# Performance work log

Hardware: AMD Instinct MI355X
Metric: run time of the kernel (lower is better)

## Reference

```python
import jax, jax.numpy as jnp
import numpy as np

HEADS = 16
ROT_DIM = 32  # RotaryEmbedding(dim=32), interleaved (GPT-J style) as in rotary_embedding_torch
THETA = 10000.0


def _rope(x):
    # x: (B, H, S, hd); rotate first ROT_DIM dims, pass through the rest
    S = x.shape[-2]
    inv_freq = 1.0 / (THETA ** (jnp.arange(0, ROT_DIM, 2, dtype=jnp.float32) / ROT_DIM))  # (ROT_DIM/2,)
    ang = jnp.arange(S, dtype=jnp.float32)[:, None] * inv_freq[None, :]                   # (S, ROT_DIM/2)
    ang = jnp.repeat(ang, 2, axis=-1)                                                     # (S, ROT_DIM) interleaved
    cos, sin = jnp.cos(ang), jnp.sin(ang)
    xr, xp = x[..., :ROT_DIM], x[..., ROT_DIM:]
    # rotate_half, interleaved pairs: (x1, x2) -> (-x2, x1)
    x2 = xr.reshape(*xr.shape[:-1], ROT_DIM // 2, 2)
    xr_half = jnp.stack([-x2[..., 1], x2[..., 0]], axis=-1).reshape(xr.shape)
    xr = xr * cos + xr_half * sin
    return jnp.concatenate([xr, xp], axis=-1)


def _split_heads(x, H):
    # (S, B, D) -> (B, H, S, hd)
    S, B, D = x.shape
    return x.transpose(1, 0, 2).reshape(B, S, H, D // H).transpose(0, 2, 1, 3)


def setup_inputs() -> dict:
    key = jax.random.key(0)
    ks = jax.random.split(key, 11)
    S, B, D = 2048, 2, 1024
    f = lambda k, shp, s=1.0: jax.random.normal(k, shp, dtype=jnp.float32) * s
    return {
        "Q": f(ks[0], (S, B, D)),
        "K": f(ks[1], (S, B, D)),
        "V": f(ks[2], (S, B, D)),
        "Wq": f(ks[3], (D, D), 0.02), "bq": f(ks[4], (D,), 0.02),
        "Wk": f(ks[5], (D, D), 0.02), "bk": f(ks[6], (D,), 0.02),
        "Wv": f(ks[7], (D, D), 0.02), "bv": f(ks[8], (D,), 0.02),
        "Wo": f(ks[9], (D, D), 0.02), "bo": f(ks[10], (D,), 0.02),
    }


def reference(Q, K, V, Wq, bq, Wk, bk, Wv, bv, Wo, bo):
    S, B, D = Q.shape
    H = HEADS
    hd = D // H
    q = _rope(_split_heads(Q @ Wq.T + bq, H))   # (B, H, S, hd)
    k = _rope(_split_heads(K @ Wk.T + bk, H))
    v = _split_heads(V @ Wv.T + bv, H)
    scores = jnp.einsum("bhqd,bhkd->bhqk", q, k) / jnp.sqrt(jnp.float32(hd))
    probs = jax.nn.softmax(scores, axis=-1)
    out = jnp.einsum("bhqk,bhkd->bhqd", probs, v)  # (B, H, S, hd)
    out = out.transpose(0, 2, 1, 3).reshape(B, S, D).transpose(1, 0, 2)  # (S, B, D)
    return out @ Wo.T + bo
```

## Files before the change

kernel.cpp:

```cpp
#include <hip/hip_runtime.h>
#include <hip/hip_bf16.h>
#include <hip/hip_fp16.h>

#define S_LEN  2048
#define BATCH  2
#define DMODEL 1024
#define NHEADS 16
#define HD     64
#define MROWS  4096
#define LD     72

using f16 = _Float16;
typedef __attribute__((ext_vector_type(8))) _Float16 f16x8;
typedef __attribute__((ext_vector_type(4))) _Float16 f16x4;
typedef __attribute__((ext_vector_type(4))) float    f32x4;

__device__ __forceinline__ void gload16(const void* g, void* l)
{
    __builtin_amdgcn_global_load_lds((const __attribute__((address_space(1))) void*)g,
                                     (__attribute__((address_space(3))) void*)l, 16, 0, 0);
}

__global__ __launch_bounds__(256) void rope_table(float* __restrict__ rc, float* __restrict__ rs)
{
    int idx = blockIdx.x * 256 + threadIdx.x;
    int s = idx >> 4, i = idx & 15;
    float inv = powf(10000.0f, -(float)(2 * i) / 32.0f);
    float ang = (float)s * inv;
    rc[idx] = cosf(ang);
    rs[idx] = sinf(ang);
}

__global__ __launch_bounds__(256) void cvt_all(
    const float* __restrict__ Q, const float* __restrict__ K, const float* __restrict__ V,
    const float* __restrict__ Wq, const float* __restrict__ Wk, const float* __restrict__ Wv,
    const float* __restrict__ Wo, f16* __restrict__ dst)
{
    const int z = blockIdx.y;
    const float* src; size_t off; int n8;
    switch (z) {
        case 0:  src = Q;  off = 0;        n8 = 524288; break;
        case 1:  src = K;  off = 4194304;  n8 = 524288; break;
        case 2:  src = V;  off = 8388608;  n8 = 524288; break;
        case 3:  src = Wq; off = 12582912; n8 = 131072; break;
        case 4:  src = Wk; off = 13631488; n8 = 131072; break;
        case 5:  src = Wv; off = 14680064; n8 = 131072; break;
        default: src = Wo; off = 15728640; n8 = 131072; break;
    }
    int i = blockIdx.x * 256 + threadIdx.x;
    if (i >= n8) return;
    const float4* s = reinterpret_cast<const float4*>(src) + (size_t)i * 2;
    float4 v0 = s[0], v1 = s[1];
    f16x8 h = { (f16)v0.x, (f16)v0.y, (f16)v0.z, (f16)v0.w,
                (f16)v1.x, (f16)v1.y, (f16)v1.z, (f16)v1.w };
    reinterpret_cast<f16x8*>(dst + off)[i] = h;
}

__global__ __launch_bounds__(256) void proj_gemm_h(
    const f16* __restrict__ Xq, const f16* __restrict__ Xk, const f16* __restrict__ Xv,
    const f16* __restrict__ Wq, const f16* __restrict__ Wk, const f16* __restrict__ Wv,
    const float* __restrict__ bq, const float* __restrict__ bk, const float* __restrict__ bv,
    f16* __restrict__ qo, f16* __restrict__ ko, f16* __restrict__ vo,
    const float* __restrict__ rc, const float* __restrict__ rs)
{
    const int mode = blockIdx.z;
    const f16* X     = (mode == 0) ? Xq : (mode == 1) ? Xk : Xv;
    const f16* W     = (mode == 0) ? Wq : (mode == 1) ? Wk : Wv;
    const float* bias = (mode == 0) ? bq : (mode == 1) ? bk : bv;

    __shared__ f16 Al[128 * 32];
    __shared__ f16 Bl[128 * 32];

    const int t = threadIdx.x, lane = t & 63, wid = t >> 6;
    const int q15 = lane & 15, g = lane >> 4;
    const int wr = wid >> 1, wc = wid & 1;
    const int m0 = blockIdx.x * 128, n0 = blockIdx.y * 128;

    const int srow = wid * 16 + (lane >> 2);
    const int scol = (lane & 3) * 8;
    const f16* Xg = X + (size_t)(m0 + srow) * DMODEL + scol;
    const f16* Wg = W + (size_t)(n0 + srow) * DMODEL + scol;
    f16* al0 = &Al[(wid * 16) * 32];
    f16* al1 = &Al[(wid * 16 + 64) * 32];
    f16* bl0 = &Bl[(wid * 16) * 32];
    f16* bl1 = &Bl[(wid * 16 + 64) * 32];

    f32x4 acc[4][4];
    #pragma unroll
    for (int m = 0; m < 4; m++)
        #pragma unroll
        for (int n = 0; n < 4; n++)
            acc[m][n] = f32x4{0.f, 0.f, 0.f, 0.f};

    for (int k0 = 0; k0 < DMODEL; k0 += 32) {
        __syncthreads();
        gload16(Xg + k0, al0);
        gload16(Xg + (size_t)64 * DMODEL + k0, al1);
        gload16(Wg + k0, bl0);
        gload16(Wg + (size_t)64 * DMODEL + k0, bl1);
        __syncthreads();

        f16x8 a[4], b[4];
        #pragma unroll
        for (int m = 0; m < 4; m++)
            a[m] = *reinterpret_cast<const f16x8*>(&Al[(wr * 64 + m * 16 + q15) * 32 + g * 8]);
        #pragma unroll
        for (int n = 0; n < 4; n++)
            b[n] = *reinterpret_cast<const f16x8*>(&Bl[(wc * 64 + n * 16 + q15) * 32 + g * 8]);
        #pragma unroll
        for (int m = 0; m < 4; m++)
            #pragma unroll
            for (int n = 0; n < 4; n++)
                acc[m][n] = __builtin_amdgcn_mfma_f32_16x16x32_f16(a[m], b[n], acc[m][n], 0, 0, 0);
    }

    const int rowb = m0 + wr * 64, colb = n0 + wc * 64;
    #pragma unroll
    for (int n = 0; n < 4; n++) {
        int cN = colb + n * 16 + q15;
        float bvv = bias[cN];
        int h = cN >> 6, d = cN & 63;
        #pragma unroll
        for (int m = 0; m < 4; m++) {
            #pragma unroll
            for (int rg = 0; rg < 4; rg++) {
                int r = rowb + m * 16 + g * 4 + rg;
                int s = r >> 1, bi = r & 1;
                float val = acc[m][n][rg] + bvv;
                if (mode < 2) {
                    float pv = __shfl_xor(val, 1);
                    if (d < 32) {
                        int fi = d >> 1;
                        float cc = rc[s * 16 + fi], ss = rs[s * 16 + fi];
                        val = ((d & 1) == 0) ? val * cc - pv * ss : val * cc + pv * ss;
                    }
                    if (mode == 0) val *= 0.18033688f;
                    ((mode == 0) ? qo : ko)[(((size_t)bi * NHEADS + h) * S_LEN + s) * HD + d] = (f16)val;
                } else {
                    vo[(((size_t)bi * NHEADS + h) * HD + d) * S_LEN + s] = (f16)val;
                }
            }
        }
    }
}

__global__ __launch_bounds__(256) void out_gemm_h(
    const f16* __restrict__ X, const f16* __restrict__ W,
    const float* __restrict__ bias, float* __restrict__ out)
{
    __shared__ f16 Al[128 * 32];
    __shared__ f16 Bl[128 * 32];

    const int t = threadIdx.x, lane = t & 63, wid = t >> 6;
    const int q15 = lane & 15, g = lane >> 4;
    const int wr = wid >> 1, wc = wid & 1;
    const int m0 = blockIdx.x * 128, n0 = blockIdx.y * 128;

    const int srow = wid * 16 + (lane >> 2);
    const int scol = (lane & 3) * 8;
    const f16* Xg = X + (size_t)(m0 + srow) * DMODEL + scol;
    const f16* Wg = W + (size_t)(n0 + srow) * DMODEL + scol;
    f16* al0 = &Al[(wid * 16) * 32];
    f16* al1 = &Al[(wid * 16 + 64) * 32];
    f16* bl0 = &Bl[(wid * 16) * 32];
    f16* bl1 = &Bl[(wid * 16 + 64) * 32];

    f32x4 acc[4][4];
    #pragma unroll
    for (int m = 0; m < 4; m++)
        #pragma unroll
        for (int n = 0; n < 4; n++)
            acc[m][n] = f32x4{0.f, 0.f, 0.f, 0.f};

    for (int k0 = 0; k0 < DMODEL; k0 += 32) {
        __syncthreads();
        gload16(Xg + k0, al0);
        gload16(Xg + (size_t)64 * DMODEL + k0, al1);
        gload16(Wg + k0, bl0);
        gload16(Wg + (size_t)64 * DMODEL + k0, bl1);
        __syncthreads();

        f16x8 a[4], b[4];
        #pragma unroll
        for (int m = 0; m < 4; m++)
            a[m] = *reinterpret_cast<const f16x8*>(&Al[(wr * 64 + m * 16 + q15) * 32 + g * 8]);
        #pragma unroll
        for (int n = 0; n < 4; n++)
            b[n] = *reinterpret_cast<const f16x8*>(&Bl[(wc * 64 + n * 16 + q15) * 32 + g * 8]);
        #pragma unroll
        for (int m = 0; m < 4; m++)
            #pragma unroll
            for (int n = 0; n < 4; n++)
                acc[m][n] = __builtin_amdgcn_mfma_f32_16x16x32_f16(a[m], b[n], acc[m][n], 0, 0, 0);
    }

    const int rowb = m0 + wr * 64, colb = n0 + wc * 64;
    #pragma unroll
    for (int n = 0; n < 4; n++) {
        int cN = colb + n * 16 + q15;
        float bvv = bias[cN];
        #pragma unroll
        for (int m = 0; m < 4; m++) {
            #pragma unroll
            for (int rg = 0; rg < 4; rg++) {
                int r = rowb + m * 16 + g * 4 + rg;
                out[(size_t)r * DMODEL + cN] = acc[m][n][rg] + bvv;
            }
        }
    }
}

__global__ __launch_bounds__(256) void proj_gemm(
    const float* __restrict__ Xq, const float* __restrict__ Xk, const float* __restrict__ Xv,
    const float* __restrict__ Wq, const float* __restrict__ Wk, const float* __restrict__ Wv,
    const float* __restrict__ bq, const float* __restrict__ bk, const float* __restrict__ bv,
    f16* __restrict__ qo, f16* __restrict__ ko, f16* __restrict__ vo,
    const float* __restrict__ rc, const float* __restrict__ rs)
{
    const int mode = blockIdx.z;
    const float* X    = (mode == 0) ? Xq : (mode == 1) ? Xk : Xv;
    const float* W    = (mode == 0) ? Wq : (mode == 1) ? Wk : Wv;
    const float* bias = (mode == 0) ? bq : (mode == 1) ? bk : bv;

    __shared__ f16 Al[128 * 40];
    __shared__ f16 Bl[128 * 40];

    const int t = threadIdx.x;
    const int lane = t & 63, wid = t >> 6;
    const int wr = wid >> 1, wc = wid & 1;
    const int m0 = blockIdx.x * 128, n0 = blockIdx.y * 128;

    f32x4 acc[4][4];
    #pragma unroll
    for (int m = 0; m < 4; m++)
        #pragma unroll
        for (int n = 0; n < 4; n++)
            acc[m][n] = f32x4{0.f, 0.f, 0.f, 0.f};

    for (int k0 = 0; k0 < DMODEL; k0 += 32) {
        __syncthreads();
        #pragma unroll
        for (int i = 0; i < 2; i++) {
            int e = (i * 256 + t) * 8;
            int r = e >> 5, c = e & 31;
            {
                const float* src = &X[(size_t)(m0 + r) * DMODEL + k0 + c];
                float4 v0 = *reinterpret_cast<const float4*>(src);
                float4 v1 = *reinterpret_cast<const float4*>(src + 4);
                f16x8 h = { (f16)v0.x, (f16)v0.y, (f16)v0.z, (f16)v0.w,
                            (f16)v1.x, (f16)v1.y, (f16)v1.z, (f16)v1.w };
                *reinterpret_cast<f16x8*>(&Al[r * 40 + c]) = h;
            }
            {
                const float* src = &W[(size_t)(n0 + r) * DMODEL + k0 + c];
                float4 v0 = *reinterpret_cast<const float4*>(src);
                float4 v1 = *reinterpret_cast<const float4*>(src + 4);
                f16x8 h = { (f16)v0.x, (f16)v0.y, (f16)v0.z, (f16)v0.w,
                            (f16)v1.x, (f16)v1.y, (f16)v1.z, (f16)v1.w };
                *reinterpret_cast<f16x8*>(&Bl[r * 40 + c]) = h;
            }
        }
        __syncthreads();
        f16x8 a[4], b[4];
        #pragma unroll
        for (int m = 0; m < 4; m++)
            a[m] = *reinterpret_cast<const f16x8*>(&Al[(wr * 64 + m * 16 + (lane & 15)) * 40 + (lane >> 4) * 8]);
        #pragma unroll
        for (int n = 0; n < 4; n++)
            b[n] = *reinterpret_cast<const f16x8*>(&Bl[(wc * 64 + n * 16 + (lane & 15)) * 40 + (lane >> 4) * 8]);
        #pragma unroll
        for (int m = 0; m < 4; m++)
            #pragma unroll
            for (int n = 0; n < 4; n++)
                acc[m][n] = __builtin_amdgcn_mfma_f32_16x16x32_f16(a[m], b[n], acc[m][n], 0, 0, 0);
    }

    const int rowb = m0 + wr * 64, colb = n0 + wc * 64;
    #pragma unroll
    for (int n = 0; n < 4; n++) {
        int cN = colb + n * 16 + (lane & 15);
        float bvv = bias[cN];
        int h = cN >> 6, d = cN & 63;
        #pragma unroll
        for (int m = 0; m < 4; m++) {
            #pragma unroll
            for (int rg = 0; rg < 4; rg++) {
                int r = rowb + m * 16 + (lane >> 4) * 4 + rg;
                int s = r >> 1, bi = r & 1;
                float val = acc[m][n][rg] + bvv;
                if (mode < 2) {
                    float pv = __shfl_xor(val, 1);
                    if (d < 32) {
                        int fi = d >> 1;
                        float cc = rc[s * 16 + fi], ss = rs[s * 16 + fi];
                        val = ((d & 1) == 0) ? val * cc - pv * ss : val * cc + pv * ss;
                    }
                    if (mode == 0) val *= 0.18033688f;
                    ((mode == 0) ? qo : ko)[(((size_t)bi * NHEADS + h) * S_LEN + s) * HD + d] = (f16)val;
                } else {
                    vo[(((size_t)bi * NHEADS + h) * HD + d) * S_LEN + s] = (f16)val;
                }
            }
        }
    }
}

__global__ __launch_bounds__(256) void out_gemm(
    const f16* __restrict__ X, const float* __restrict__ W,
    const float* __restrict__ bias, float* __restrict__ out)
{
    __shared__ f16 Al[128 * 40];
    __shared__ f16 Bl[128 * 40];

    const int t = threadIdx.x;
    const int lane = t & 63, wid = t >> 6;
    const int wr = wid >> 1, wc = wid & 1;
    const int m0 = blockIdx.x * 128, n0 = blockIdx.y * 128;

    f32x4 acc[4][4];
    #pragma unroll
    for (int m = 0; m < 4; m++)
        #pragma unroll
        for (int n = 0; n < 4; n++)
            acc[m][n] = f32x4{0.f, 0.f, 0.f, 0.f};

    for (int k0 = 0; k0 < DMODEL; k0 += 32) {
        __syncthreads();
        #pragma unroll
        for (int i = 0; i < 2; i++) {
            int e = (i * 256 + t) * 8;
            int r = e >> 5, c = e & 31;
            *reinterpret_cast<uint4*>(&Al[r * 40 + c]) =
                *reinterpret_cast<const uint4*>(&X[(size_t)(m0 + r) * DMODEL + k0 + c]);
            {
                const float* src = &W[(size_t)(n0 + r) * DMODEL + k0 + c];
                float4 v0 = *reinterpret_cast<const float4*>(src);
                float4 v1 = *reinterpret_cast<const float4*>(src + 4);
                f16x8 h = { (f16)v0.x, (f16)v0.y, (f16)v0.z, (f16)v0.w,
                            (f16)v1.x, (f16)v1.y, (f16)v1.z, (f16)v1.w };
                *reinterpret_cast<f16x8*>(&Bl[r * 40 + c]) = h;
            }
        }
        __syncthreads();
        f16x8 a[4], b[4];
        #pragma unroll
        for (int m = 0; m < 4; m++)
            a[m] = *reinterpret_cast<const f16x8*>(&Al[(wr * 64 + m * 16 + (lane & 15)) * 40 + (lane >> 4) * 8]);
        #pragma unroll
        for (int n = 0; n < 4; n++)
            b[n] = *reinterpret_cast<const f16x8*>(&Bl[(wc * 64 + n * 16 + (lane & 15)) * 40 + (lane >> 4) * 8]);
        #pragma unroll
        for (int m = 0; m < 4; m++)
            #pragma unroll
            for (int n = 0; n < 4; n++)
                acc[m][n] = __builtin_amdgcn_mfma_f32_16x16x32_f16(a[m], b[n], acc[m][n], 0, 0, 0);
    }

    const int rowb = m0 + wr * 64, colb = n0 + wc * 64;
    #pragma unroll
    for (int n = 0; n < 4; n++) {
        int cN = colb + n * 16 + (lane & 15);
        float bvv = bias[cN];
        #pragma unroll
        for (int m = 0; m < 4; m++) {
            #pragma unroll
            for (int rg = 0; rg < 4; rg++) {
                int r = rowb + m * 16 + (lane >> 4) * 4 + rg;
                out[(size_t)r * DMODEL + cN] = acc[m][n][rg] + bvv;
            }
        }
    }
}

__global__ __launch_bounds__(512) void attn_fwd(
    const f16* __restrict__ qb, const f16* __restrict__ kb,
    const f16* __restrict__ vt, f16* __restrict__ ctx)
{
    __shared__ f16 Kl[2][64 * 64];
    __shared__ f16 Vl[2][64 * 64];
    __shared__ f16 Pl[8 * 16 * LD];

    const int t = threadIdx.x, lane = t & 63, wid = t >> 6;
    const int q15 = lane & 15, g = lane >> 4;
    const int sw = q15 & 7;
    const int bh = blockIdx.y;
    const int q0 = blockIdx.x * 128 + wid * 16;

    const f16* qptr = qb + ((size_t)bh * S_LEN + q0) * HD;
    f16x8 qf0 = *reinterpret_cast<const f16x8*>(&qptr[q15 * HD + g * 8]);
    f16x8 qf1 = *reinterpret_cast<const f16x8*>(&qptr[q15 * HD + g * 8 + 32]);

    f32x4 ctxa[4];
    #pragma unroll
    for (int i = 0; i < 4; i++) ctxa[i] = f32x4{0.f, 0.f, 0.f, 0.f};
    float mrun = -3.0e38f, lrun = 0.f;

    const int srow = t >> 3;
    const int sslot = (t & 7) ^ (srow & 7);
    const f16* kg = kb + (size_t)bh * S_LEN * HD + (size_t)srow * HD + sslot * 8;
    const f16* vg = vt + (size_t)bh * HD * S_LEN + (size_t)srow * S_LEN + sslot * 8;
    const int lds_wbase = wid * 512;
    f16* pbase = &Pl[wid * (16 * LD)];

    gload16(kg, &Kl[0][lds_wbase]);
    gload16(vg, &Vl[0][lds_wbase]);
    __syncthreads();
    int cur = 0;

    for (int kt = 0; kt < S_LEN / 64; kt++) {
        if (kt + 1 < S_LEN / 64) {
            gload16(kg + (size_t)(kt + 1) * 64 * HD, &Kl[cur ^ 1][lds_wbase]);
            gload16(vg + (size_t)(kt + 1) * 64,      &Vl[cur ^ 1][lds_wbase]);
        }
        const f16* Kc = Kl[cur];
        const f16* Vc = Vl[cur];

        f32x4 sc[4];
        __builtin_amdgcn_s_setprio(1);
        #pragma unroll
        for (int f = 0; f < 4; f++) {
            f16x8 kf0 = *reinterpret_cast<const f16x8*>(&Kc[(f * 16 + q15) * 64 + ((g ^ sw) * 8)]);
            f16x8 kf1 = *reinterpret_cast<const f16x8*>(&Kc[(f * 16 + q15) * 64 + (((g + 4) ^ sw) * 8)]);
            f32x4 z = {0.f, 0.f, 0.f, 0.f};
            z = __builtin_amdgcn_mfma_f32_16x16x32_f16(kf0, qf0, z, 0, 0, 0);
            sc[f] = __builtin_amdgcn_mfma_f32_16x16x32_f16(kf1, qf1, z, 0, 0, 0);
        }
        __builtin_amdgcn_s_setprio(0);

        float pmf[4];
        #pragma unroll
        for (int f = 0; f < 4; f++)
            pmf[f] = fmaxf(fmaxf(sc[f][0], sc[f][1]), fmaxf(sc[f][2], sc[f][3]));
        float pm = fmaxf(fmaxf(pmf[0], pmf[1]), fmaxf(pmf[2], pmf[3]));
        if (!__all(pm - mrun <= 8.0f)) {
            float pmax = fmaxf(pm, __shfl_xor(pm, 16));
            pmax = fmaxf(pmax, __shfl_xor(pmax, 32));
            float mnew = fmaxf(mrun, pmax);
            float scale = __builtin_amdgcn_exp2f(mrun - mnew);
            lrun *= scale;
            #pragma unroll
            for (int n = 0; n < 4; n++) {
                ctxa[n][0] *= scale; ctxa[n][1] *= scale;
                ctxa[n][2] *= scale; ctxa[n][3] *= scale;
            }
            mrun = mnew;
        }
        float tsum = 0.f;
        #pragma unroll
        for (int f = 0; f < 4; f++)
            #pragma unroll
            for (int rg = 0; rg < 4; rg++) {
                float p = __builtin_amdgcn_exp2f(sc[f][rg] - mrun);
                sc[f][rg] = p;
                tsum += p;
            }
        lrun += tsum;

        #pragma unroll
        for (int f = 0; f < 4; f++) {
            f16x4 pw = { (f16)sc[f][0], (f16)sc[f][1], (f16)sc[f][2], (f16)sc[f][3] };
            *reinterpret_cast<f16x4*>(&pbase[q15 * LD + f * 16 + g * 4]) = pw;
        }
        asm volatile("s_waitcnt lgkmcnt(0)" ::: "memory");
        __builtin_amdgcn_sched_barrier(0);

        __builtin_amdgcn_s_setprio(1);
        #pragma unroll
        for (int c = 0; c < 2; c++) {
            f16x8 pfr = *reinterpret_cast<const f16x8*>(&pbase[q15 * LD + g * 8 + c * 32]);
            #pragma unroll
            for (int n = 0; n < 4; n++) {
                f16x8 vf = *reinterpret_cast<const f16x8*>(&Vc[(n * 16 + q15) * 64 + (((g + c * 4) ^ sw) * 8)]);
                ctxa[n] = __builtin_amdgcn_mfma_f32_16x16x32_f16(vf, pfr, ctxa[n], 0, 0, 0);
            }
        }
        __builtin_amdgcn_s_setprio(0);

        __syncthreads();
        cur ^= 1;
    }

    lrun += __shfl_xor(lrun, 16);
    lrun += __shfl_xor(lrun, 32);
    const int bi = bh >> 4, h = bh & 15;
    const int s = q0 + q15;
    float inv = 1.0f / lrun;
    f16* outp = &ctx[((size_t)s * BATCH + bi) * DMODEL + h * HD];
    #pragma unroll
    for (int n = 0; n < 4; n++) {
        f16x4 o = { (f16)(ctxa[n][0] * inv), (f16)(ctxa[n][1] * inv),
                    (f16)(ctxa[n][2] * inv), (f16)(ctxa[n][3] * inv) };
        *reinterpret_cast<f16x4*>(&outp[n * 16 + g * 4]) = o;
    }
}

extern "C" void kernel_launch(void* const* d_in, const int* in_sizes, int n_in,
                              void* d_out, int out_size, void* d_ws, size_t ws_size,
                              hipStream_t stream)
{
    const float* Q  = (const float*)d_in[0];
    const float* K  = (const float*)d_in[1];
    const float* V  = (const float*)d_in[2];
    const float* Wq = (const float*)d_in[3];
    const float* bq = (const float*)d_in[4];
    const float* Wk = (const float*)d_in[5];
    const float* bk = (const float*)d_in[6];
    const float* Wv = (const float*)d_in[7];
    const float* bv = (const float*)d_in[8];
    const float* Wo = (const float*)d_in[9];
    const float* bo = (const float*)d_in[10];
    float* out = (float*)d_out;

    char* w = (char*)d_ws;
    const size_t MBc = 1024 * 1024;
    const size_t NEED_FAST = 56 * MBc + 256 * 1024;

    if (ws_size >= NEED_FAST) {
        f16* cvtb = (f16*)w;
        f16* Xqh = cvtb;
        f16* Xkh = cvtb + 4194304;
        f16* Xvh = cvtb + 8388608;
        f16* Wqh = cvtb + 12582912;
        f16* Wkh = cvtb + 13631488;
        f16* Wvh = cvtb + 14680064;
        f16* Woh = cvtb + 15728640;
        float* rc = (float*)(w + 32 * MBc);
        float* rs = rc + 32768;
        f16* qbuf = (f16*)(w + 32 * MBc + 256 * 1024);
        f16* kbuf = qbuf + 4194304;
        f16* vtb  = kbuf + 4194304;
        f16* ctxb = Xqh;

        rope_table<<<(S_LEN * 16) / 256, 256, 0, stream>>>(rc, rs);
        cvt_all<<<dim3(2048, 7), 256, 0, stream>>>(Q, K, V, Wq, Wk, Wv, Wo, cvtb);
        proj_gemm_h<<<dim3(MROWS / 128, DMODEL / 128, 3), 256, 0, stream>>>(
            Xqh, Xkh, Xvh, Wqh, Wkh, Wvh, bq, bk, bv, qbuf, kbuf, vtb, rc, rs);
        attn_fwd<<<dim3(S_LEN / 128, BATCH * NHEADS), 512, 0, stream>>>(qbuf, kbuf, vtb, ctxb);
        out_gemm_h<<<dim3(MROWS / 128, DMODEL / 128), 256, 0, stream>>>(ctxb, Woh, bo, out);
    } else {
        const size_t szT = (size_t)S_LEN * 16 * sizeof(float);
        const size_t szQ = (size_t)MROWS * DMODEL * sizeof(f16);
        float* rc  = (float*)(w);
        float* rs  = (float*)(w + szT);
        f16* qbuf = (f16*)(w + 2 * szT);
        f16* kbuf = (f16*)(w + 2 * szT + szQ);
        f16* vtb  = (f16*)(w + 2 * szT + 2 * szQ);
        f16* ctxb = (f16*)(w + 2 * szT + 3 * szQ);

        rope_table<<<(S_LEN * 16) / 256, 256, 0, stream>>>(rc, rs);
        proj_gemm<<<dim3(MROWS / 128, DMODEL / 128, 3), 256, 0, stream>>>(
            Q, K, V, Wq, Wk, Wv, bq, bk, bv, qbuf, kbuf, vtb, rc, rs);
        attn_fwd<<<dim3(S_LEN / 128, BATCH * NHEADS), 512, 0, stream>>>(qbuf, kbuf, vtb, ctxb);
        out_gemm<<<dim3(MROWS / 128, DMODEL / 128), 256, 0, stream>>>(ctxb, Wo, bo, out);
    }
}
```

Measured before the change: 150.8 us.

## Software-pipeline attention so PV of previous tile overlaps QK of current

Restructures the attention inner loop so the P·V MFMAs for tile kt-1 are issued right after the Q·K MFMAs for tile kt, with a final epilogue for the last tile. V gets a third LDS buffer and P gets a second buffer so the previous tile's data stays live across the sync. This removes the explicit lgkmcnt wait and the serial dependency between writing P and reading it back in the same iteration, giving the scheduler more independent MFMA work to hide softmax latency. In exchange, LDS use per block grows, which could reduce occupancy, and register pressure may rise.

```diff
diff --git a/kernel.cpp b/kernel.cpp
--- a/kernel.cpp
+++ b/kernel.cpp
@@ -9,6 +9,7 @@
 #define HD     64
 #define MROWS  4096
 #define LD     72
+#define NT     (S_LEN / 64)
 
 using f16 = _Float16;
 typedef __attribute__((ext_vector_type(8))) _Float16 f16x8;
@@ -377,8 +378,8 @@
     const f16* __restrict__ vt, f16* __restrict__ ctx)
 {
     __shared__ f16 Kl[2][64 * 64];
-    __shared__ f16 Vl[2][64 * 64];
-    __shared__ f16 Pl[8 * 16 * LD];
+    __shared__ f16 Vl[3][64 * 64];
+    __shared__ f16 Pl[2][8 * 16 * LD];
 
     const int t = threadIdx.x, lane = t & 63, wid = t >> 6;
     const int q15 = lane & 15, g = lane >> 4;
@@ -400,20 +401,21 @@
     const f16* kg = kb + (size_t)bh * S_LEN * HD + (size_t)srow * HD + sslot * 8;
     const f16* vg = vt + (size_t)bh * HD * S_LEN + (size_t)srow * S_LEN + sslot * 8;
     const int lds_wbase = wid * 512;
-    f16* pbase = &Pl[wid * (16 * LD)];
+    const int poff = wid * (16 * LD);
 
     gload16(kg, &Kl[0][lds_wbase]);
     gload16(vg, &Vl[0][lds_wbase]);
     __syncthreads();
-    int cur = 0;
-
-    for (int kt = 0; kt < S_LEN / 64; kt++) {
-        if (kt + 1 < S_LEN / 64) {
-            gload16(kg + (size_t)(kt + 1) * 64 * HD, &Kl[cur ^ 1][lds_wbase]);
-            gload16(vg + (size_t)(kt + 1) * 64,      &Vl[cur ^ 1][lds_wbase]);
-        }
-        const f16* Kc = Kl[cur];
-        const f16* Vc = Vl[cur];
+
+    int kbuf = 0;
+    int vprev = 2, vcur = 0, vnext = 1;
+
+    for (int kt = 0; kt < NT; kt++) {
+        if (kt + 1 < NT) {
+            gload16(kg + (size_t)(kt + 1) * 64 * HD, &Kl[kbuf ^ 1][lds_wbase]);
+            gload16(vg + (size_t)(kt + 1) * 64,      &Vl[vnext][lds_wbase]);
+        }
+        const f16* Kc = Kl[kbuf];
 
         f32x4 sc[4];
         __builtin_amdgcn_s_setprio(1);
@@ -424,6 +426,19 @@
             f32x4 z = {0.f, 0.f, 0.f, 0.f};
             z = __builtin_amdgcn_mfma_f32_16x16x32_f16(kf0, qf0, z, 0, 0, 0);
             sc[f] = __builtin_amdgcn_mfma_f32_16x16x32_f16(kf1, qf1, z, 0, 0, 0);
+        }
+        if (kt > 0) {
+            const f16* Vp = Vl[vprev];
+            const f16* pr = &Pl[(kt & 1) ^ 1][poff];
+            #pragma unroll
+            for (int c = 0; c < 2; c++) {
+                f16x8 pfr = *reinterpret_cast<const f16x8*>(&pr[q15 * LD + g * 8 + c * 32]);
+                #pragma unroll
+                for (int n = 0; n < 4; n++) {
+                    f16x8 vf = *reinterpret_cast<const f16x8*>(&Vp[(n * 16 + q15) * 64 + (((g + c * 4) ^ sw) * 8)]);
+                    ctxa[n] = __builtin_amdgcn_mfma_f32_16x16x32_f16(vf, pfr, ctxa[n], 0, 0, 0);
+                }
+            }
         }
         __builtin_amdgcn_s_setprio(0);
 
@@ -456,28 +471,30 @@
             }
         lrun += tsum;
 
+        f16* pw = &Pl[kt & 1][poff];
         #pragma unroll
         for (int f = 0; f < 4; f++) {
-            f16x4 pw = { (f16)sc[f][0], (f16)sc[f][1], (f16)sc[f][2], (f16)sc[f][3] };
-            *reinterpret_cast<f16x4*>(&pbase[q15 * LD + f * 16 + g * 4]) = pw;
-        }
-        asm volatile("s_waitcnt lgkmcnt(0)" ::: "memory");
-        __builtin_amdgcn_sched_barrier(0);
-
-        __builtin_amdgcn_s_setprio(1);
+            f16x4 pwv = { (f16)sc[f][0], (f16)sc[f][1], (f16)sc[f][2], (f16)sc[f][3] };
+            *reinterpret_cast<f16x4*>(&pw[q15 * LD + f * 16 + g * 4]) = pwv;
+        }
+
+        __syncthreads();
+        kbuf ^= 1;
+        int tmp = vprev; vprev = vcur; vcur = vnext; vnext = tmp;
+    }
+
+    {
+        const f16* Vp = Vl[vprev];
+        const f16* pr = &Pl[(NT - 1) & 1][poff];
         #pragma unroll
         for (int c = 0; c < 2; c++) {
-            f16x8 pfr = *reinterpret_cast<const f16x8*>(&pbase[q15 * LD + g * 8 + c * 32]);
+            f16x8 pfr = *reinterpret_cast<const f16x8*>(&pr[q15 * LD + g * 8 + c * 32]);
             #pragma unroll
             for (int n = 0; n < 4; n++) {
-                f16x8 vf = *reinterpret_cast<const f16x8*>(&Vc[(n * 16 + q15) * 64 + (((g + c * 4) ^ sw) * 8)]);
+                f16x8 vf = *reinterpret_cast<const f16x8*>(&Vp[(n * 16 + q15) * 64 + (((g + c * 4) ^ sw) * 8)]);
                 ctxa[n] = __builtin_amdgcn_mfma_f32_16x16x32_f16(vf, pfr, ctxa[n], 0, 0, 0);
             }
         }
-        __builtin_amdgcn_s_setprio(0);
-
-        __syncthreads();
-        cur ^= 1;
     }
 
     lrun += __shfl_xor(lrun, 16);
```

After: 150.5 us. Within noise of the previous version (-0.2%).
